# Optimization experiments

Hardware: AMD Instinct MI355X
Metric: run time of the kernel (lower is better)

The kernel has to match this reference:

```python
import jax, jax.numpy as jnp
import numpy as np

D = 768       # model dim (mha.input_dim)
M = 16        # memory tokens
S = 1024      # input sequence length
B = 16        # batch
SCALE = 1.0 / np.sqrt(D).astype(np.float32)  # mha.scaling


def setup_inputs() -> dict:
    key = jax.random.key(0)
    ks = jax.random.split(key, 11)
    x = jax.random.normal(ks[0], (B, S, D), dtype=jnp.float32)
    mask = jnp.zeros((S, S + M), dtype=jnp.float32)  # additive mask over [q_len, kv_len]
    memory = jax.random.normal(ks[1], (1, M, D), dtype=jnp.float32) * 0.02
    wq = jax.random.normal(ks[2], (D, D), dtype=jnp.float32) / np.sqrt(D)
    bq = jnp.zeros((D,), dtype=jnp.float32)
    wk = jax.random.normal(ks[3], (D, D), dtype=jnp.float32) / np.sqrt(D)
    bk = jnp.zeros((D,), dtype=jnp.float32)
    wv = jax.random.normal(ks[4], (D, D), dtype=jnp.float32) / np.sqrt(D)
    bv = jnp.zeros((D,), dtype=jnp.float32)
    wo = jax.random.normal(ks[5], (D, D), dtype=jnp.float32) / np.sqrt(D)
    bo = jnp.zeros((D,), dtype=jnp.float32)
    return {"x": x, "mask": mask, "memory": memory,
            "wq": wq, "bq": bq, "wk": wk, "bk": bk,
            "wv": wv, "bv": bv, "wo": wo, "bo": bo}


def reference(x, mask, memory, wq, bq, wk, bk, wv, bv, wo, bo):
    # concat learnable memory tokens onto the key/value stream
    mem = jnp.broadcast_to(memory, (x.shape[0], M, D))
    kv_in = jnp.concatenate([x, mem], axis=1)            # [B, S+M, D]
    q = jnp.einsum('bsd,ed->bse', x, wq) + bq            # [B, S,   D]
    k = jnp.einsum('btd,ed->bte', kv_in, wk) + bk        # [B, S+M, D]
    v = jnp.einsum('btd,ed->bte', kv_in, wv) + bv        # [B, S+M, D]
    scores = jnp.einsum('bse,bte->bst', q, k) * SCALE    # [B, S, S+M]
    attn = jax.nn.softmax(scores + mask, axis=-1)
    head_out = jnp.einsum('bst,bte->bse', attn, v)       # [B, S, D]
    attended = jnp.einsum('bse,fe->bsf', head_out, wo) + bo
    return attended[:, :S, :]                            # split(...)[0]: first S tokens
```

## Files before the change

### kernel.cpp

```cpp
#include <hip/hip_runtime.h>
#include <math.h>
#include <stdint.h>

#define D_    768
#define B_    16
#define S_    1024
#define M_    16
#define SM_   1040
#define SMP_  1088
#define SCALE_ 0.036084392f

typedef __bf16 bf16;
typedef __attribute__((ext_vector_type(8))) __bf16 bf16x8;
typedef __attribute__((ext_vector_type(4))) __bf16 bf16x4;
typedef __attribute__((ext_vector_type(4))) float  f32x4;

#define GL16(gp, lp) __builtin_amdgcn_global_load_lds( \
    (const __attribute__((address_space(1))) void*)(gp), \
    (__attribute__((address_space(3))) void*)(lp), 16, 0, 0)

template<int OUTMODE, int GM>
__launch_bounds__(256, 3)
__global__ void gemm_k(const bf16*  __restrict__ Am,
                       const bf16*  __restrict__ Bm,
                       const float* __restrict__ aux,
                       void* __restrict__ Cout,
                       void* __restrict__ C2,
                       void* __restrict__ C3,
                       int lda, int ldb, int ldc,
                       int K, int colsB,
                       long sA, long sB, long sC)
{
    __shared__ __attribute__((aligned(16))) bf16 As[128 * 64];
    __shared__ __attribute__((aligned(16))) bf16 Bs[128 * 64];

    const int t    = threadIdx.x;
    const int l    = t & 63;
    const int wv   = t >> 6;

    int row0, col0, z;
    if (GM == 1) {
        const int bid = blockIdx.x;
        const int xcd = bid & 7, s = bid >> 3;
        z = xcd * 2 + s / 72;
        const int r = s % 72;
        row0 = (r & 7) * 128; col0 = (r >> 3) * 128;
    } else if (GM == 2) {
        const int bid = blockIdx.x;
        const int xcd = bid & 7, s = bid >> 3;
        z = xcd * 2 + s / 48;
        const int r = s % 48;
        row0 = (r & 7) * 128; col0 = (r >> 3) * 128;
    } else {
        row0 = blockIdx.y * 128; col0 = blockIdx.x * 128; z = 0;
    }

    const bf16* agb[4];
    const bf16* bgb[4];
    #pragma unroll
    for (int i = 0; i < 4; ++i) {
        const int r = (wv * 4 + i) * 8 + (l >> 3);
        const int c = (l & 7) ^ (r & 7);
        agb[i] = Am + (size_t)z * sA + (size_t)(row0 + r) * lda + c * 8;
        int bcol = col0 + r;
        if (bcol > colsB - 1) bcol = colsB - 1;
        bgb[i] = Bm + (size_t)z * sB + (size_t)bcol * ldb + c * 8;
    }

    f32x4 acc[4][4];
    #pragma unroll
    for (int i = 0; i < 4; ++i)
        #pragma unroll
        for (int j = 0; j < 4; ++j)
            acc[i][j] = (f32x4){0.f, 0.f, 0.f, 0.f};

    const int wr0 = (wv & 1) * 64;
    const int wc0 = (wv >> 1) * 64;
    const int lq  = l >> 4;
    const int lm  = l & 15;

    for (int kt = 0; kt < K; kt += 64) {
        __syncthreads();
        #pragma unroll
        for (int i = 0; i < 4; ++i)
            GL16(agb[i] + kt, &As[(wv * 4 + i) * 512]);
        #pragma unroll
        for (int i = 0; i < 4; ++i)
            GL16(bgb[i] + kt, &Bs[(wv * 4 + i) * 512]);
        __syncthreads();

        #pragma unroll
        for (int ks = 0; ks < 2; ++ks) {
            bf16x8 af[4], bfr[4];
            #pragma unroll
            for (int i = 0; i < 4; ++i) {
                const int rowA = wr0 + i * 16 + lm;
                const int p = (ks * 4 + lq) ^ (rowA & 7);
                af[i] = *(const bf16x8*)&As[rowA * 64 + p * 8];
            }
            #pragma unroll
            for (int j = 0; j < 4; ++j) {
                const int rowB = wc0 + j * 16 + lm;
                const int p = (ks * 4 + lq) ^ (rowB & 7);
                bfr[j] = *(const bf16x8*)&Bs[rowB * 64 + p * 8];
            }
            #pragma unroll
            for (int i = 0; i < 4; ++i)
                #pragma unroll
                for (int j = 0; j < 4; ++j)
                    acc[i][j] = __builtin_amdgcn_mfma_f32_16x16x32_bf16(
                        af[i], bfr[j], acc[i][j], 0, 0, 0);
        }
    }

    if (OUTMODE == 4) {
        const bf16* em = (const bf16*)C3;
        float* rsum = (float*)C2;
        #pragma unroll
        for (int i = 0; i < 4; ++i) {
            const int t0 = row0 + wr0 + i * 16 + lq * 4;
            #pragma unroll
            for (int r = 0; r < 4; ++r) {
                float part = 0.f;
                #pragma unroll
                for (int j = 0; j < 4; ++j) {
                    const int gcol = col0 + wc0 + j * 16 + lm;
                    float val = 0.f;
                    if (gcol < SM_)
                        val = __expf(acc[i][j][r])
                            * (float)em[(size_t)(t0 + r) * SM_ + gcol];
                    const bf16 vb = (bf16)val;
                    part += (float)vb;
                    if (gcol < SMP_)
                        ((bf16*)Cout)[(size_t)z * sC
                            + (size_t)(t0 + r) * ldc + gcol] = vb;
                }
                #pragma unroll
                for (int o = 8; o; o >>= 1) part += __shfl_xor(part, o);
                if (lm == 0)
                    atomicAdd(&rsum[z * S_ + t0 + r], part);
            }
        }
        return;
    }

    float rin[4][4];
    if (OUTMODE == 5) {
        #pragma unroll
        for (int i = 0; i < 4; ++i) {
            const int t0 = row0 + wr0 + i * 16 + lq * 4;
            #pragma unroll
            for (int r = 0; r < 4; ++r)
                rin[i][r] = 1.f / aux[z * S_ + t0 + r];
        }
    }

    const int wsel = (OUTMODE == 3) ? (col0 / 768) : 0;
    #pragma unroll
    for (int j = 0; j < 4; ++j) {
        const int gcol = col0 + wc0 + j * 16 + lm;
        #pragma unroll
        for (int i = 0; i < 4; ++i) {
            const int t0 = row0 + wr0 + i * 16 + lq * 4;
            if (OUTMODE == 3) {
                const int lcol = gcol - wsel * 768;
                const float bv = aux[gcol];
                const int b  = t0 / SM_;
                const int tt = t0 - b * SM_;
                if (wsel == 0) {
                    if (tt < S_) {
                        #pragma unroll
                        for (int r = 0; r < 4; ++r)
                            ((bf16*)Cout)[((size_t)b * S_ + tt + r) * D_ + lcol]
                                = (bf16)(acc[i][j][r] + bv);
                    }
                } else if (wsel == 1) {
                    #pragma unroll
                    for (int r = 0; r < 4; ++r)
                        ((bf16*)C2)[(size_t)(t0 + r) * D_ + lcol]
                            = (bf16)(acc[i][j][r] + bv);
                } else {
                    bf16x4 o;
                    #pragma unroll
                    for (int r = 0; r < 4; ++r) o[r] = (bf16)(acc[i][j][r] + bv);
                    *(bf16x4*)((bf16*)C3 +
                        ((size_t)b * D_ + lcol) * SMP_ + tt) = o;
                }
            } else if (OUTMODE == 5) {
                #pragma unroll
                for (int r = 0; r < 4; ++r)
                    ((bf16*)Cout)[(size_t)z * sC + (size_t)(t0 + r) * ldc + gcol]
                        = (bf16)(acc[i][j][r] * rin[i][r]);
            } else {
                if (gcol < colsB) {
                    const float bv = aux ? aux[gcol] : 0.f;
                    #pragma unroll
                    for (int r = 0; r < 4; ++r)
                        ((float*)Cout)[(size_t)z * sC
                            + (size_t)(t0 + r) * ldc + gcol]
                            = acc[i][j][r] + bv;
                }
            }
        }
    }
}

__global__ void castw4_k(const float* __restrict__ w0, const float* __restrict__ w1,
                         const float* __restrict__ w2, const float* __restrict__ w3,
                         bf16* __restrict__ wqkv, bf16* __restrict__ wob)
{
    const float* in;
    bf16* out;
    float sc = 1.f;
    const size_t NW = (size_t)D_ * D_;
    switch (blockIdx.y) {
        case 0: in = w0; out = wqkv;          sc = SCALE_; break;
        case 1: in = w1; out = wqkv + NW;     break;
        case 2: in = w2; out = wqkv + 2 * NW; break;
        default: in = w3; out = wob;          break;
    }
    const int i = blockIdx.x * blockDim.x + threadIdx.x;
    const float4 f = ((const float4*)in)[i];
    bf16x4 v;
    v[0] = (bf16)(f.x * sc); v[1] = (bf16)(f.y * sc);
    v[2] = (bf16)(f.z * sc); v[3] = (bf16)(f.w * sc);
    ((bf16x4*)out)[i] = v;
}

__global__ void emask_k(const float* __restrict__ mask, bf16* __restrict__ em)
{
    const int i = blockIdx.x * blockDim.x + threadIdx.x;
    const float4 f = ((const float4*)mask)[i];
    bf16x4 v;
    v[0] = (bf16)__expf(f.x); v[1] = (bf16)__expf(f.y);
    v[2] = (bf16)__expf(f.z); v[3] = (bf16)__expf(f.w);
    ((bf16x4*)em)[i] = v;
}

__global__ void castx_k(const float* __restrict__ x, const float* __restrict__ mem,
                        bf16* __restrict__ cs,
                        const float* __restrict__ bq, const float* __restrict__ bk,
                        const float* __restrict__ bv, float* __restrict__ bqkv,
                        float* __restrict__ rsum)
{
    if (blockIdx.x == 6240) {
        const int tid = threadIdx.x;
        if (tid < 576) {
            const int g = tid * 4;
            float4 f;
            if (g < 768) {
                f = *(const float4*)(bq + g);
                f.x *= SCALE_; f.y *= SCALE_; f.z *= SCALE_; f.w *= SCALE_;
            } else if (g < 1536) {
                f = *(const float4*)(bk + g - 768);
            } else {
                f = *(const float4*)(bv + g - 1536);
            }
            *(float4*)(bqkv + g) = f;
        }
        const float4 zz = make_float4(0.f, 0.f, 0.f, 0.f);
        #pragma unroll
        for (int k = 0; k < 16; ++k)
            *(float4*)(rsum + tid * 64 + k * 4) = zz;
        return;
    }
    const int i = blockIdx.x * blockDim.x + threadIdx.x;
    const int row = i / 96;
    const int c8  = (i - row * 96) * 8;
    const int b   = row / SM_;
    const int tt  = row - b * SM_;
    const float* src = (tt < S_) ? (x + ((size_t)b * S_ + tt) * D_ + c8)
                                 : (mem + (size_t)(tt - S_) * D_ + c8);
    const float4 f0 = *(const float4*)src;
    const float4 f1 = *(const float4*)(src + 4);
    bf16x8 v;
    v[0] = (bf16)f0.x; v[1] = (bf16)f0.y; v[2] = (bf16)f0.z; v[3] = (bf16)f0.w;
    v[4] = (bf16)f1.x; v[5] = (bf16)f1.y; v[6] = (bf16)f1.z; v[7] = (bf16)f1.w;
    *(bf16x8*)(cs + (size_t)row * D_ + c8) = v;
}

extern "C" void kernel_launch(void* const* d_in, const int* in_sizes, int n_in,
                              void* d_out, int out_size, void* d_ws, size_t ws_size,
                              hipStream_t stream) {
    const float* x    = (const float*)d_in[0];
    const float* mask = (const float*)d_in[1];
    const float* mem  = (const float*)d_in[2];
    const float* wq   = (const float*)d_in[3];
    const float* bq   = (const float*)d_in[4];
    const float* wk   = (const float*)d_in[5];
    const float* bk   = (const float*)d_in[6];
    const float* wv   = (const float*)d_in[7];
    const float* bv   = (const float*)d_in[8];
    const float* wo   = (const float*)d_in[9];
    const float* bo   = (const float*)d_in[10];

    bf16* w = (bf16*)d_ws;
    const size_t NW  = (size_t)D_ * D_;
    const size_t NCS = (size_t)B_ * SM_ * D_;
    const size_t NQ  = (size_t)B_ * S_ * D_;
    const size_t NKV = (size_t)B_ * SM_ * D_;
    const size_t NVT = (size_t)B_ * D_ * SMP_;
    const size_t NEM = (size_t)S_ * SM_;
    bf16* wqkv = w;
    bf16* wob  = wqkv + 3 * NW;
    bf16* emb  = wob + NW;
    bf16* cs   = emb + NEM;
    bf16* qb   = cs  + NCS;
    bf16* kb   = qb  + NQ;
    bf16* vtb  = kb  + NKV;
    bf16* Pb   = vtb + NVT;
    float* bqkv = (float*)(Pb + (size_t)B_ * S_ * SMP_);
    float* rsum = bqkv + 2304;

    castw4_k<<<dim3(576, 4), 256, 0, stream>>>(wq, wk, wv, wo, wqkv, wob);
    emask_k<<<1040, 256, 0, stream>>>(mask, emb);
    castx_k<<<6241, 256, 0, stream>>>(x, mem, cs, bq, bk, bv, bqkv, rsum);

    gemm_k<3, 3><<<dim3(18, 130), 256, 0, stream>>>(
        cs, wqkv, bqkv, qb, kb, vtb, D_, D_, 0, D_, 3 * D_, 0, 0, 0);

    gemm_k<4, 1><<<1152, 256, 0, stream>>>(
        qb, kb, nullptr, Pb, rsum, emb, D_, D_, SMP_, D_, SM_,
        (long)S_ * D_, (long)SM_ * D_, (long)S_ * SMP_);

    gemm_k<5, 2><<<768, 256, 0, stream>>>(
        Pb, vtb, rsum, cs, nullptr, nullptr, SMP_, SMP_, D_, SMP_, D_,
        (long)S_ * SMP_, (long)D_ * SMP_, (long)S_ * D_);

    gemm_k<1, 3><<<dim3(6, 128), 256, 0, stream>>>(
        cs, wob, bo, d_out, nullptr, nullptr, D_, D_, D_, D_, D_, 0, 0, 0);
}
```

Measured before the change: 339.1 us.

## Rewrite GEMM as 256x256 tile, 8-wave double-buffered pipelined kernel

Replaces the 128x128, 4-wave, single-buffered GEMM with a 256x256 tile on 8 waves (512 threads). It double-buffers LDS and issues staged global-to-LDS loads for the next k-tiles while MFMAs on the current tile run, using explicit waitcnt, barriers and setprio. The larger tiles cut global traffic per FLOP, but they cost more LDS (128KB) and registers, leave fewer blocks per grid (e.g. 192 for PV), and add tile-quantisation waste on the 1040/1088 dimensions.

```diff
diff --git a/kernel.cpp b/kernel.cpp
--- a/kernel.cpp
+++ b/kernel.cpp
@@ -20,114 +20,166 @@
     (__attribute__((address_space(3))) void*)(lp), 16, 0, 0)
 
 template<int OUTMODE, int GM>
-__launch_bounds__(256, 3)
-__global__ void gemm_k(const bf16*  __restrict__ Am,
-                       const bf16*  __restrict__ Bm,
-                       const float* __restrict__ aux,
-                       void* __restrict__ Cout,
-                       void* __restrict__ C2,
-                       void* __restrict__ C3,
-                       int lda, int ldb, int ldc,
-                       int K, int colsB,
-                       long sA, long sB, long sC)
+__launch_bounds__(512, 2)
+__global__ void gemm8_k(const bf16*  __restrict__ Am,
+                        const bf16*  __restrict__ Bm,
+                        const float* __restrict__ aux,
+                        void* __restrict__ Cout,
+                        void* __restrict__ C2,
+                        void* __restrict__ C3,
+                        int lda, int ldb, int ldc,
+                        int K, int colsB,
+                        long sA, long sB, long sC)
 {
-    __shared__ __attribute__((aligned(16))) bf16 As[128 * 64];
-    __shared__ __attribute__((aligned(16))) bf16 Bs[128 * 64];
-
-    const int t    = threadIdx.x;
-    const int l    = t & 63;
-    const int wv   = t >> 6;
+    __shared__ __attribute__((aligned(16))) bf16 As[2][256 * 64];
+    __shared__ __attribute__((aligned(16))) bf16 Bs[2][256 * 64];
+
+    const int t   = threadIdx.x;
+    const int l   = t & 63;
+    const int wvi = t >> 6;
+    const int wm  = wvi >> 2;
+    const int wn  = wvi & 3;
+    const int lq  = l >> 4;
+    const int lm  = l & 15;
+    const int l8  = l >> 3;
+    const int csw = ((l & 7) ^ l8) * 8;
 
     int row0, col0, z;
     if (GM == 1) {
         const int bid = blockIdx.x;
         const int xcd = bid & 7, s = bid >> 3;
-        z = xcd * 2 + s / 72;
-        const int r = s % 72;
-        row0 = (r & 7) * 128; col0 = (r >> 3) * 128;
+        z = xcd * 2 + s / 20;
+        const int r = s % 20;
+        row0 = (r & 3) * 256; col0 = (r >> 2) * 256;
     } else if (GM == 2) {
         const int bid = blockIdx.x;
         const int xcd = bid & 7, s = bid >> 3;
-        z = xcd * 2 + s / 48;
-        const int r = s % 48;
-        row0 = (r & 7) * 128; col0 = (r >> 3) * 128;
+        z = xcd * 2 + s / 12;
+        const int r = s % 12;
+        row0 = z * 1024 + (r % 4) * 256; col0 = (r / 4) * 256;
     } else {
-        row0 = blockIdx.y * 128; col0 = blockIdx.x * 128; z = 0;
-    }
-
-    const bf16* agb[4];
-    const bf16* bgb[4];
+        row0 = blockIdx.y * 256; col0 = blockIdx.x * 256; z = 0;
+    }
+
+    const bf16* aL = Am + (size_t)((GM == 2) ? 0 : z) * sA
+                        + (size_t)(row0 + l8) * lda + csw;
+    const bf16* bZ = Bm + (size_t)z * sB + csw;
+
+    auto stageA = [&](int h, int buf, int kt) {
+        #pragma unroll
+        for (int q = 0; q < 2; ++q) {
+            const int u  = wvi * 2 + q;
+            const int rb = (u & 7) * 8 + (u >> 3) * 128 + h * 64;
+            GL16(aL + (size_t)rb * lda + kt, &As[buf][rb * 64]);
+        }
+    };
+    auto stageB = [&](int h, int buf, int kt) {
+        #pragma unroll
+        for (int q = 0; q < 2; ++q) {
+            const int u  = wvi * 2 + q;
+            const int rb = (u & 3) * 8 + (u >> 2) * 64 + h * 32;
+            int bc = col0 + rb + l8;
+            if (bc > colsB - 1) bc = colsB - 1;
+            GL16(bZ + (size_t)bc * ldb + kt, &Bs[buf][rb * 64]);
+        }
+    };
+
+    f32x4 acc[8][4];
     #pragma unroll
-    for (int i = 0; i < 4; ++i) {
-        const int r = (wv * 4 + i) * 8 + (l >> 3);
-        const int c = (l & 7) ^ (r & 7);
-        agb[i] = Am + (size_t)z * sA + (size_t)(row0 + r) * lda + c * 8;
-        int bcol = col0 + r;
-        if (bcol > colsB - 1) bcol = colsB - 1;
-        bgb[i] = Bm + (size_t)z * sB + (size_t)bcol * ldb + c * 8;
-    }
-
-    f32x4 acc[4][4];
-    #pragma unroll
-    for (int i = 0; i < 4; ++i)
-        #pragma unroll
-        for (int j = 0; j < 4; ++j)
-            acc[i][j] = (f32x4){0.f, 0.f, 0.f, 0.f};
-
-    const int wr0 = (wv & 1) * 64;
-    const int wc0 = (wv >> 1) * 64;
-    const int lq  = l >> 4;
-    const int lm  = l & 15;
-
-    for (int kt = 0; kt < K; kt += 64) {
-        __syncthreads();
-        #pragma unroll
-        for (int i = 0; i < 4; ++i)
-            GL16(agb[i] + kt, &As[(wv * 4 + i) * 512]);
-        #pragma unroll
-        for (int i = 0; i < 4; ++i)
-            GL16(bgb[i] + kt, &Bs[(wv * 4 + i) * 512]);
-        __syncthreads();
-
-        #pragma unroll
-        for (int ks = 0; ks < 2; ++ks) {
-            bf16x8 af[4], bfr[4];
+    for (int m = 0; m < 8; ++m)
+        #pragma unroll
+        for (int n = 0; n < 4; ++n)
+            acc[m][n] = (f32x4){0.f, 0.f, 0.f, 0.f};
+
+    bf16x8 aq[4][2], b0[2][2], b1[2][2];
+
+    auto rdA = [&](bf16x8 (&dst)[4][2], int mbase, int buf) {
+        #pragma unroll
+        for (int mm = 0; mm < 4; ++mm)
             #pragma unroll
-            for (int i = 0; i < 4; ++i) {
-                const int rowA = wr0 + i * 16 + lm;
-                const int p = (ks * 4 + lq) ^ (rowA & 7);
-                af[i] = *(const bf16x8*)&As[rowA * 64 + p * 8];
-            }
+            for (int ks = 0; ks < 2; ++ks) {
+                const int row = wm * 128 + (mbase + mm) * 16 + lm;
+                const int p   = (ks * 4 + lq) ^ (row & 7);
+                dst[mm][ks] = *(const bf16x8*)&As[buf][row * 64 + p * 8];
+            }
+    };
+    auto rdB = [&](bf16x8 (&dst)[2][2], int nbase, int buf) {
+        #pragma unroll
+        for (int nn = 0; nn < 2; ++nn)
             #pragma unroll
-            for (int j = 0; j < 4; ++j) {
-                const int rowB = wc0 + j * 16 + lm;
-                const int p = (ks * 4 + lq) ^ (rowB & 7);
-                bfr[j] = *(const bf16x8*)&Bs[rowB * 64 + p * 8];
-            }
-            #pragma unroll
-            for (int i = 0; i < 4; ++i)
-                #pragma unroll
-                for (int j = 0; j < 4; ++j)
-                    acc[i][j] = __builtin_amdgcn_mfma_f32_16x16x32_bf16(
-                        af[i], bfr[j], acc[i][j], 0, 0, 0);
-        }
-    }
+            for (int ks = 0; ks < 2; ++ks) {
+                const int row = wn * 64 + (nbase + nn) * 16 + lm;
+                const int p   = (ks * 4 + lq) ^ (row & 7);
+                dst[nn][ks] = *(const bf16x8*)&Bs[buf][row * 64 + p * 8];
+            }
+    };
+
+    #define MMA4x2(mb, nb, a, b) { \
+        _Pragma("unroll") for (int ks = 0; ks < 2; ++ks) \
+        _Pragma("unroll") for (int mm = 0; mm < 4; ++mm) \
+        _Pragma("unroll") for (int nn = 0; nn < 2; ++nn) \
+            acc[(mb)+mm][(nb)+nn] = __builtin_amdgcn_mfma_f32_16x16x32_bf16( \
+                a[mm][ks], b[nn][ks], acc[(mb)+mm][(nb)+nn], 0, 0, 0); }
+
+    const int nT = K >> 6;
+
+    stageA(0, 0, 0);  stageB(0, 0, 0);  stageB(1, 0, 0);  stageA(1, 0, 0);
+    stageA(0, 1, 64); stageB(0, 1, 64); stageB(1, 1, 64);
+    asm volatile("s_waitcnt vmcnt(6)" ::: "memory");
+    __builtin_amdgcn_s_barrier();
+
+    for (int kt8 = 0; kt8 < nT; ++kt8) {
+        const int bc = kt8 & 1, bn = bc ^ 1;
+        const int kt1 = (kt8 + 1) << 6, kt2 = (kt8 + 2) << 6;
+        rdA(aq, 0, bc); rdB(b0, 0, bc);
+        if (kt8 + 1 < nT) stageA(1, bn, kt1);
+        __builtin_amdgcn_s_barrier();
+        asm volatile("s_waitcnt lgkmcnt(0)" ::: "memory");
+        __builtin_amdgcn_s_setprio(1);
+        MMA4x2(0, 0, aq, b0);
+        __builtin_amdgcn_s_setprio(0);
+        __builtin_amdgcn_s_barrier();
+        rdB(b1, 2, bc);
+        if (kt8 + 2 < nT) stageA(0, bc, kt2);
+        __builtin_amdgcn_s_barrier();
+        asm volatile("s_waitcnt lgkmcnt(0)" ::: "memory");
+        __builtin_amdgcn_s_setprio(1);
+        MMA4x2(0, 2, aq, b1);
+        __builtin_amdgcn_s_setprio(0);
+        __builtin_amdgcn_s_barrier();
+        rdA(aq, 4, bc);
+        if (kt8 + 2 < nT) stageB(0, bc, kt2);
+        __builtin_amdgcn_s_barrier();
+        asm volatile("s_waitcnt lgkmcnt(0)" ::: "memory");
+        __builtin_amdgcn_s_setprio(1);
+        MMA4x2(4, 0, aq, b0);
+        __builtin_amdgcn_s_setprio(0);
+        __builtin_amdgcn_s_barrier();
+        if (kt8 + 2 < nT) stageB(1, bc, kt2);
+        __builtin_amdgcn_s_setprio(1);
+        MMA4x2(4, 2, aq, b1);
+        __builtin_amdgcn_s_setprio(0);
+        if (kt8 >= nT - 2) asm volatile("s_waitcnt vmcnt(0)" ::: "memory");
+        else               asm volatile("s_waitcnt vmcnt(6)" ::: "memory");
+        __builtin_amdgcn_s_barrier();
+    }
+    #undef MMA4x2
 
     if (OUTMODE == 4) {
         const bf16* em = (const bf16*)C3;
         float* rsum = (float*)C2;
         #pragma unroll
-        for (int i = 0; i < 4; ++i) {
-            const int t0 = row0 + wr0 + i * 16 + lq * 4;
+        for (int m = 0; m < 8; ++m) {
+            const int t0 = row0 + wm * 128 + m * 16 + lq * 4;
             #pragma unroll
             for (int r = 0; r < 4; ++r) {
                 float part = 0.f;
                 #pragma unroll
-                for (int j = 0; j < 4; ++j) {
-                    const int gcol = col0 + wc0 + j * 16 + lm;
+                for (int n = 0; n < 4; ++n) {
+                    const int gcol = col0 + wn * 64 + n * 16 + lm;
                     float val = 0.f;
                     if (gcol < SM_)
-                        val = __expf(acc[i][j][r])
+                        val = __expf(acc[m][n][r])
                             * (float)em[(size_t)(t0 + r) * SM_ + gcol];
                     const bf16 vb = (bf16)val;
                     part += (float)vb;
@@ -144,61 +196,60 @@
         return;
     }
 
-    float rin[4][4];
+    float rin[8][4];
     if (OUTMODE == 5) {
         #pragma unroll
-        for (int i = 0; i < 4; ++i) {
-            const int t0 = row0 + wr0 + i * 16 + lq * 4;
+        for (int m = 0; m < 8; ++m) {
+            const int t0 = row0 + wm * 128 + m * 16 + lq * 4;
             #pragma unroll
             for (int r = 0; r < 4; ++r)
-                rin[i][r] = 1.f / aux[z * S_ + t0 + r];
+                rin[m][r] = 1.f / aux[t0 + r];
         }
     }
 
     const int wsel = (OUTMODE == 3) ? (col0 / 768) : 0;
     #pragma unroll
-    for (int j = 0; j < 4; ++j) {
-        const int gcol = col0 + wc0 + j * 16 + lm;
-        #pragma unroll
-        for (int i = 0; i < 4; ++i) {
-            const int t0 = row0 + wr0 + i * 16 + lq * 4;
+    for (int n = 0; n < 4; ++n) {
+        const int gcol = col0 + wn * 64 + n * 16 + lm;
+        #pragma unroll
+        for (int m = 0; m < 8; ++m) {
+            const int t0 = row0 + wm * 128 + m * 16 + lq * 4;
             if (OUTMODE == 3) {
                 const int lcol = gcol - wsel * 768;
                 const float bv = aux[gcol];
                 const int b  = t0 / SM_;
-                const int tt = t0 - b * SM_;
+                const int tb = t0 - b * SM_;
                 if (wsel == 0) {
-                    if (tt < S_) {
+                    if (tb < S_) {
                         #pragma unroll
                         for (int r = 0; r < 4; ++r)
-                            ((bf16*)Cout)[((size_t)b * S_ + tt + r) * D_ + lcol]
-                                = (bf16)(acc[i][j][r] + bv);
+                            ((bf16*)Cout)[((size_t)b * S_ + tb + r) * D_ + lcol]
+                                = (bf16)(acc[m][n][r] + bv);
                     }
                 } else if (wsel == 1) {
                     #pragma unroll
                     for (int r = 0; r < 4; ++r)
                         ((bf16*)C2)[(size_t)(t0 + r) * D_ + lcol]
-                            = (bf16)(acc[i][j][r] + bv);
+                            = (bf16)(acc[m][n][r] + bv);
                 } else {
                     bf16x4 o;
                     #pragma unroll
-                    for (int r = 0; r < 4; ++r) o[r] = (bf16)(acc[i][j][r] + bv);
+                    for (int r = 0; r < 4; ++r) o[r] = (bf16)(acc[m][n][r] + bv);
                     *(bf16x4*)((bf16*)C3 +
-                        ((size_t)b * D_ + lcol) * SMP_ + tt) = o;
+                        ((size_t)b * D_ + lcol) * SMP_ + tb) = o;
                 }
             } else if (OUTMODE == 5) {
                 #pragma unroll
                 for (int r = 0; r < 4; ++r)
-                    ((bf16*)Cout)[(size_t)z * sC + (size_t)(t0 + r) * ldc + gcol]
-                        = (bf16)(acc[i][j][r] * rin[i][r]);
+                    ((bf16*)Cout)[(size_t)(t0 + r) * ldc + gcol]
+                        = (bf16)(acc[m][n][r] * rin[m][r]);
             } else {
                 if (gcol < colsB) {
                     const float bv = aux ? aux[gcol] : 0.f;
                     #pragma unroll
                     for (int r = 0; r < 4; ++r)
-                        ((float*)Cout)[(size_t)z * sC
-                            + (size_t)(t0 + r) * ldc + gcol]
-                            = acc[i][j][r] + bv;
+                        ((float*)Cout)[(size_t)(t0 + r) * ldc + gcol]
+                            = acc[m][n][r] + bv;
                 }
             }
         }
@@ -316,17 +367,17 @@
     emask_k<<<1040, 256, 0, stream>>>(mask, emb);
     castx_k<<<6241, 256, 0, stream>>>(x, mem, cs, bq, bk, bv, bqkv, rsum);
 
-    gemm_k<3, 3><<<dim3(18, 130), 256, 0, stream>>>(
+    gemm8_k<3, 3><<<dim3(9, 65), 512, 0, stream>>>(
         cs, wqkv, bqkv, qb, kb, vtb, D_, D_, 0, D_, 3 * D_, 0, 0, 0);
 
-    gemm_k<4, 1><<<1152, 256, 0, stream>>>(
+    gemm8_k<4, 1><<<320, 512, 0, stream>>>(
         qb, kb, nullptr, Pb, rsum, emb, D_, D_, SMP_, D_, SM_,
         (long)S_ * D_, (long)SM_ * D_, (long)S_ * SMP_);
 
-    gemm_k<5, 2><<<768, 256, 0, stream>>>(
+    gemm8_k<5, 2><<<192, 512, 0, stream>>>(
         Pb, vtb, rsum, cs, nullptr, nullptr, SMP_, SMP_, D_, SMP_, D_,
-        (long)S_ * SMP_, (long)D_ * SMP_, (long)S_ * D_);
-
-    gemm_k<1, 3><<<dim3(6, 128), 256, 0, stream>>>(
+        0, (long)D_ * SMP_, 0);
+
+    gemm8_k<1, 3><<<dim3(3, 64), 512, 0, stream>>>(
         cs, wob, bo, d_out, nullptr, nullptr, D_, D_, D_, D_, D_, 0, 0, 0);
 }
```

After: 413.8 us. 22.0% more time.
